# Kernel optimization log

Measured on AMD Instinct MI355X. Metric: run time of the kernel, lower is better.

Reference implementation:

```python
import jax, jax.numpy as jnp
import numpy as np

# ---- real Clebsch-Gordon tensors (Wigner 3j up to norm/sign) via equivariance null-space ----
def _su2_gens(l):
    m = np.arange(-l, l + 1)
    Lz = np.diag(m).astype(complex)
    c = np.sqrt(l * (l + 1) - m[:-1] * (m[:-1] + 1))
    Lp = np.zeros((2 * l + 1, 2 * l + 1), complex)
    Lp[np.arange(1, 2 * l + 1), np.arange(2 * l)] = c
    Lm = Lp.conj().T
    return (Lp + Lm) / 2, (Lp - Lm) / 2j, Lz

def _q_real(l):
    # complex -> real spherical-harmonic change of basis
    Q = np.zeros((2 * l + 1, 2 * l + 1), complex)
    s2 = np.sqrt(2.0)
    for m in range(-l, l + 1):
        i = m + l
        if m == 0:
            Q[i, l] = 1.0
        elif m > 0:
            Q[i, l + m] = (-1.0) ** m / s2
            Q[i, l - m] = 1.0 / s2
        else:
            Q[i, l + m] = 1j / s2
            Q[i, l - m] = -1j * (-1.0) ** m / s2
    return Q

def _real_gens(l):
    Q = _q_real(l)
    return [np.real(Q @ (1j * L) @ Q.conj().T) for L in _su2_gens(l)]

_CG = {}
def clebsch_gordon(l1, l2, l3):
    key = (l1, l2, l3)
    if key not in _CG:
        n1, n2, n3 = 2 * l1 + 1, 2 * l2 + 1, 2 * l3 + 1
        G = [_real_gens(l) for l in (l1, l2, l3)]
        rows = []
        for a in range(3):
            rows.append(np.kron(G[0][a], np.eye(n2 * n3))
                        + np.kron(np.eye(n1), np.kron(G[1][a], np.eye(n3)))
                        + np.kron(np.eye(n1 * n2), G[2][a]))
        _, s, Vh = np.linalg.svd(np.concatenate(rows, 0))
        v = Vh[-1]  # unique invariant vector (unit norm)
        if v[np.argmax(np.abs(v))] < 0:
            v = -v
        _CG[key] = v.reshape(n1, n2, n3).astype(np.float32)
    return _CG[key]

# ---- static irreps configuration (mul, degree l, parity p) ----
TP_L = [(32, 0, 1), (32, 1, -1)]
TP_R = [(32, 0, 1), (32, 1, -1)]
IRREPS_IN = [(128, 0, 1), (128, 1, -1), (128, 1, 1), (128, 2, 1)]
B = 8192
D_IN = sum(m * (2 * l + 1) for m, l, _ in IRREPS_IN)  # 1536

def _key(l, p):
    return f"{l}{'e' if p == 1 else 'o'}"

def _build_out_irreps():
    mul, order = {}, []
    for ml, ll, pl in TP_L:
        for mr, lr, pr in TP_R:
            p = pl * pr
            for l in range(abs(ll - lr), ll + lr + 1):
                k = _key(l, p)
                if k not in mul:
                    mul[k] = 0
                    order.append((l, p))
                mul[k] += ml * mr
    return [(mul[_key(l, p)], l, p) for (l, p) in order]

IRREPS_OUT = _build_out_irreps()  # [(2048,0,1),(2048,1,-1),(1024,1,1),(1024,2,1)]

def _build_schedule():
    # replicates the original's tail-consuming slice logic per (pair, output irrep)
    starts, off = [], 0
    for mul, l, p in IRREPS_OUT:
        starts.append(off)
        off += mul * (2 * l + 1)
    rem = {_key(l, p): mul for mul, l, p in IRREPS_OUT}
    sched = []
    for ml, ll, pl in TP_L:
        for mr, lr, pr in TP_R:
            mul = ml * mr
            terms = []
            for i, (mo, l, p) in enumerate(IRREPS_OUT):
                if p != pl * pr or not (abs(ll - lr) <= l <= ll + lr):
                    continue
                k = _key(l, p)
                stop = starts[i] + rem[k] * (2 * l + 1)
                start = stop - mul * (2 * l + 1)
                rem[k] -= mul
                terms.append((start, stop, l, clebsch_gordon(ll, lr, l)))
            sched.append((ml, ll, mr, lr, terms))
    assert all(v == 0 for v in rem.values())
    return sched, off

SCHEDULE, D_OUT = _build_schedule()  # D_OUT == 16384

def setup_inputs() -> dict:
    key = jax.random.key(0)
    ks = jax.random.split(key, 5)
    x = jax.random.normal(ks[0], (B, D_IN), jnp.float32)
    w_0e = jax.random.normal(ks[1], (128, 2048), jnp.float32) / np.sqrt(128.0)
    w_1o = jax.random.normal(ks[2], (128, 2048), jnp.float32) / np.sqrt(128.0)
    w_1e = jax.random.normal(ks[3], (128, 1024), jnp.float32) / np.sqrt(128.0)
    w_2e = jax.random.normal(ks[4], (128, 1024), jnp.float32) / np.sqrt(128.0)
    return {"x": x, "w_0e": w_0e, "w_1o": w_1o, "w_1e": w_1e, "w_2e": w_2e}

def _linear(x, ws):
    # e3nn-style PointwiseLinear: mix multiplicities within each irrep type
    in_off, off = {}, 0
    for m, l, p in IRREPS_IN:
        in_off[_key(l, p)] = (off, m)
        off += m * (2 * l + 1)
    outs = []
    for (mo, l, p), w in zip(IRREPS_OUT, ws):
        o, mi = in_off[_key(l, p)]
        d = 2 * l + 1
        xi = x[:, o:o + mi * d].reshape(-1, mi, d)  # [B, mul_in, 2l+1]
        yo = jnp.einsum('bui,uv->bvi', xi, w)       # [B, mul_out, 2l+1]
        outs.append(yo.reshape(xi.shape[0], mo * d))
    return jnp.concatenate(outs, axis=1)  # [B, D_OUT]

def reference(x, w_0e, w_1o, w_1e, w_2e):
    y = _linear(x, (w_0e, w_1o, w_1e, w_2e))
    blocks = []
    for ml, ll, mr, lr, terms in SCHEDULE:
        acc = None
        for start, stop, l, cg in terms:
            a = y[:, start:stop].reshape(-1, ml, mr, 2 * l + 1)  # [B,mul_l,mul_r,2l+1]
            t = jnp.einsum('bmni,lri->bmlnr', a, jnp.asarray(cg))
            acc = t if acc is None else acc + t  # [B,mul_l,2ll+1,mul_r,2lr+1]
        blocks.append(acc.reshape(acc.shape[0], -1))
    return jnp.concatenate(blocks, axis=1)  # [B, 16384]
```

## Files before the change

### kernel.cpp

```cpp
#include <hip/hip_runtime.h>


typedef __attribute__((ext_vector_type(8))) __bf16 bf16x8;
typedef __attribute__((ext_vector_type(8))) unsigned short u16x8;
typedef __attribute__((ext_vector_type(4))) float f32x4;
typedef __attribute__((ext_vector_type(2))) float f32x2;

#define A_V8_TOTAL (12 * 512 * 4 * 64)
#define B_V8_TOTAL (384 * 4 * 64)
#define P_STRIDE   (512 * 4 * 64)
#define WS_NEED_BYTES ((size_t)(A_V8_TOTAL + B_V8_TOTAL) * 16)

__device__ __forceinline__ unsigned short f2bf(float f) {
  unsigned u = __builtin_bit_cast(unsigned, f);
  u = (u + 0x7FFFu + ((u >> 16) & 1u)) >> 16;
  return (unsigned short)u;
}

__device__ __forceinline__ f32x4 mfma16(bf16x8 a, bf16x8 b, f32x4 c) {
  return __builtin_amdgcn_mfma_f32_16x16x32_bf16(a, b, c, 0, 0, 0);
}
__device__ __forceinline__ bf16x8 asbf(u16x8 v) { return __builtin_bit_cast(bf16x8, v); }
__device__ __forceinline__ void stnt(float* p, float v) { __builtin_nontemporal_store(v, p); }
__device__ __forceinline__ void stnt2(float* p, float a, float b) {
  f32x2 v; v[0] = a; v[1] = b;
  __builtin_nontemporal_store(v, (f32x2*)p);
}

__device__ __forceinline__ void gload_lds16(const void* g, void* s) {
  __builtin_amdgcn_global_load_lds((const __attribute__((address_space(1))) void*)g,
                                   (__attribute__((address_space(3))) void*)s, 16, 0, 0);
}

__global__ __launch_bounds__(256) void prep_kernel(
    const float* __restrict__ x, const float* __restrict__ w0e,
    const float* __restrict__ w1o, const float* __restrict__ w1e,
    const float* __restrict__ w2e, u16x8* __restrict__ ws) {
  int t = blockIdx.x * 256 + threadIdx.x;
  if (t < A_V8_TOTAL) {
    int l = t & 63;
    int kb = (t >> 6) & 3;
    int mt = (t >> 8) & 511;
    int p = t >> 17;
    int m = mt * 16 + (l & 15);
    int k0 = kb * 32 + (l >> 4) * 8;
    int base, d, comp;
    if (p == 0)      { base = 0;   d = 1; comp = 0;     }
    else if (p < 4)  { base = 128; d = 3; comp = p - 1; }
    else if (p < 7)  { base = 512; d = 3; comp = p - 4; }
    else             { base = 896; d = 5; comp = p - 7; }
    const float* xr = x + (size_t)m * 1536 + base + comp + k0 * d;
    u16x8 v;
#pragma unroll
    for (int e = 0; e < 8; ++e) v[e] = f2bf(xr[e * d]);
    ws[t] = v;
  } else {
    int tb = t - A_V8_TOTAL;
    if (tb >= B_V8_TOTAL) return;
    int l = tb & 63;
    int kb = (tb >> 6) & 3;
    int ci = tb >> 8;
    const float* w; int N, v0;
    if (ci < 128)      { w = w0e; N = 2048; v0 = ci * 16;         }
    else if (ci < 256) { w = w1o; N = 2048; v0 = (ci - 128) * 16; }
    else if (ci < 320) { w = w1e; N = 1024; v0 = (ci - 256) * 16; }
    else               { w = w2e; N = 1024; v0 = (ci - 320) * 16; }
    int n = v0 + (l & 15);
    int k0 = kb * 32 + (l >> 4) * 8;
    u16x8 v;
#pragma unroll
    for (int e = 0; e < 8; ++e) v[e] = f2bf(w[(size_t)(k0 + e) * N + n]);
    ws[A_V8_TOTAL + tb] = v;
  }
}

#define CLS_OF(p) ((p) == 0 ? 0 : (p) < 4 ? 1 : (p) < 7 ? 2 : 3)

__global__ __launch_bounds__(256) void tp_main(const u16x8* __restrict__ ws,
                                               float* __restrict__ out) {
  __shared__ __align__(16) u16x8 Ash[2][1536];
  const int tid = threadIdx.x;
  const int l = tid & 63;
  const int wv = tid >> 6;
  const int bid = blockIdx.x;
  const int logical = (bid & 7) * 768 + (bid >> 3);
  const int mt2 = logical / 24;
  const int sub = logical - mt2 * 24;
  const int l15 = l & 15, lhi = l >> 4;
  const u16x8* Ap = ws;
  const u16x8* Bp = ws + A_V8_TOTAL;
  const bool isL = sub < 8;
  const int nstage = isL ? 6 : 2;

  const float c3  = 0.57735026918962576f;
  const float c6  = 0.40824829046386302f;
  const float c10 = 0.31622776601683794f;
  const float c30 = 0.18257418583505537f;

  auto stageA = [&](int kb, int buf) {
    for (int i = 0; i < nstage; ++i) {
      const int e = i * 256 + tid;
      const int p = e >> 7, mfi = (e >> 6) & 1;
      const u16x8* src = Ap + (size_t)p * P_STRIDE +
                         (((((mt2 << 1) | mfi) << 2) + kb) << 6) + (e & 63);
      gload_lds16(src, &Ash[buf][i * 256 + (tid & 192)]);
    }
  };

  stageA(0, 0);

  if (isL) {
    const int vq = sub * 4 + wv;
    f32x4 acc[2][2][12];
#pragma unroll
    for (int mf = 0; mf < 2; ++mf)
#pragma unroll
      for (int vh = 0; vh < 2; ++vh)
#pragma unroll
        for (int p = 0; p < 12; ++p) acc[mf][vh][p] = (f32x4)(0.0f);

    int buf = 0;
#pragma unroll
    for (int kb = 0; kb < 4; ++kb) {
      __syncthreads();
      if (kb < 3) stageA(kb + 1, buf ^ 1);
      bf16x8 b[2][4];
#pragma unroll
      for (int vh = 0; vh < 2; ++vh) {
        const int vt = vq * 2 + vh;
        b[vh][0] = asbf(Bp[(((vt)       << 2) + kb) * 64 + l]);
        b[vh][1] = asbf(Bp[(((128 + vt) << 2) + kb) * 64 + l]);
        b[vh][2] = asbf(Bp[(((256 + vt) << 2) + kb) * 64 + l]);
        b[vh][3] = asbf(Bp[(((320 + vt) << 2) + kb) * 64 + l]);
      }
#pragma unroll
      for (int mf = 0; mf < 2; ++mf) {
        const u16x8* af = &Ash[buf][mf * 64 + l];
#pragma unroll
        for (int p = 0; p < 12; ++p) {
          const bf16x8 a = asbf(af[p * 128]);
          acc[mf][0][p] = mfma16(a, b[0][CLS_OF(p)], acc[mf][0][p]);
          acc[mf][1][p] = mfma16(a, b[1][CLS_OF(p)], acc[mf][1][p]);
        }
      }
      buf ^= 1;
    }
    const int v5 = vq;
#pragma unroll
    for (int vh = 0; vh < 2; ++vh) {
      const int v31 = (vh << 4) | l15;
#pragma unroll
      for (int mf = 0; mf < 2; ++mf) {
#pragma unroll
        for (int j = 0; j < 4; ++j) {
          const int m = mt2 * 32 + mf * 16 + lhi * 4 + j;
          float* orow = out + (size_t)m * 16384;
          float* oc = orow + 4096 + v5 * 96 + v31;
          stnt(oc + 0,  acc[mf][vh][1][j] * c3);
          stnt(oc + 32, acc[mf][vh][2][j] * c3);
          stnt(oc + 64, acc[mf][vh][3][j] * c3);
          const float s  = acc[mf][vh][0][j] * c3;
          const float e0 = acc[mf][vh][4][j], e1 = acc[mf][vh][5][j], e2 = acc[mf][vh][6][j];
          const float q0 = acc[mf][vh][7][j], q1 = acc[mf][vh][8][j];
          const float q2 = acc[mf][vh][9][j], q3 = acc[mf][vh][10][j], q4 = acc[mf][vh][11][j];
          float* od = orow + 7168 + v5 * 288 + v31 * 3;
          stnt2(od + 0,   s - q2 * c30 - q4 * c10,
                          -e2 * c6 + q1 * c10);
          stnt (od + 2,   e1 * c6 + q0 * c10);
          stnt2(od + 96,  e2 * c6 + q1 * c10,
                          s + 2.0f * q2 * c30);
          stnt (od + 98,  -e0 * c6 + q3 * c10);
          stnt2(od + 192, -e1 * c6 + q0 * c10,
                          e0 * c6 + q3 * c10);
          stnt (od + 194, s - q2 * c30 + q4 * c10);
        }
      }
    }
  } else {
    const int vtp = (sub - 8) * 4 + wv;
    f32x4 acc[2][4];
#pragma unroll
    for (int mf = 0; mf < 2; ++mf)
#pragma unroll
      for (int p = 0; p < 4; ++p) acc[mf][p] = (f32x4)(0.0f);

    const int ci0 = 64 + vtp, ci1 = 192 + vtp;
    int buf = 0;
#pragma unroll
    for (int kb = 0; kb < 4; ++kb) {
      __syncthreads();
      if (kb < 3) stageA(kb + 1, buf ^ 1);
      bf16x8 b0 = asbf(Bp[((ci0 << 2) + kb) * 64 + l]);
      bf16x8 b1 = asbf(Bp[((ci1 << 2) + kb) * 64 + l]);
#pragma unroll
      for (int mf = 0; mf < 2; ++mf) {
        const u16x8* af = &Ash[buf][mf * 64 + l];
        acc[mf][0] = mfma16(asbf(af[0 * 128]), b0, acc[mf][0]);
        acc[mf][1] = mfma16(asbf(af[1 * 128]), b1, acc[mf][1]);
        acc[mf][2] = mfma16(asbf(af[2 * 128]), b1, acc[mf][2]);
        acc[mf][3] = mfma16(asbf(af[3 * 128]), b1, acc[mf][3]);
      }
      buf ^= 1;
    }
    const int vp = vtp * 16 + l15;
#pragma unroll
    for (int mf = 0; mf < 2; ++mf) {
#pragma unroll
      for (int j = 0; j < 4; ++j) {
        const int m = mt2 * 32 + mf * 16 + lhi * 4 + j;
        float* orow = out + (size_t)m * 16384;
        stnt(orow + vp, acc[mf][0][j]);
        float* ob = orow + 1024 + vp * 3;
        stnt2(ob + 0, acc[mf][1][j] * c3, acc[mf][2][j] * c3);
        stnt (ob + 2, acc[mf][3][j] * c3);
      }
    }
  }
}

extern "C" void kernel_launch(void* const* d_in, const int* in_sizes, int n_in,
                              void* d_out, int out_size, void* d_ws, size_t ws_size,
                              hipStream_t stream) {
  if (ws_size < WS_NEED_BYTES) return;
  const float* x   = (const float*)d_in[0];
  const float* w0e = (const float*)d_in[1];
  const float* w1o = (const float*)d_in[2];
  const float* w1e = (const float*)d_in[3];
  const float* w2e = (const float*)d_in[4];
  u16x8* ws = (u16x8*)d_ws;
  float* out = (float*)d_out;

  prep_kernel<<<6528, 256, 0, stream>>>(x, w0e, w1o, w1e, w2e, ws);
  tp_main<<<6144, 256, 0, stream>>>(ws, out);
}
```

Before: 145.0 us.

## Merge light and heavy tensor-product work into each block, cut grid to 2048

Each block used to run either the heavy l=1 output path or the light path (0e/1o outputs), chosen by sub-index across 6144 blocks. Now every block runs the heavy path and then the light path for the same row tile, and the light path doubles its per-wave column width to two vh halves. The intent is to remove the load imbalance between block types and reduce launch and A-staging count. The cost is longer blocks with more sequential work, re-staging of A for the second phase, and possibly higher register pressure.

After: 150.3 us. 1.04x slower.

```diff
diff --git a/kernel.cpp b/kernel.cpp
--- a/kernel.cpp
+++ b/kernel.cpp
@@ -83,21 +83,19 @@
   const int l = tid & 63;
   const int wv = tid >> 6;
   const int bid = blockIdx.x;
-  const int logical = (bid & 7) * 768 + (bid >> 3);
-  const int mt2 = logical / 24;
-  const int sub = logical - mt2 * 24;
+  const int logical = (bid & 7) * 256 + (bid >> 3);
+  const int mt2 = logical >> 3;
+  const int vq = ((logical & 7) << 2) | wv;
   const int l15 = l & 15, lhi = l >> 4;
   const u16x8* Ap = ws;
   const u16x8* Bp = ws + A_V8_TOTAL;
-  const bool isL = sub < 8;
-  const int nstage = isL ? 6 : 2;
 
   const float c3  = 0.57735026918962576f;
   const float c6  = 0.40824829046386302f;
   const float c10 = 0.31622776601683794f;
   const float c30 = 0.18257418583505537f;
 
-  auto stageA = [&](int kb, int buf) {
+  auto stageA = [&](int kb, int buf, int nstage) {
     for (int i = 0; i < nstage; ++i) {
       const int e = i * 256 + tid;
       const int p = e >> 7, mfi = (e >> 6) & 1;
@@ -107,10 +105,8 @@
     }
   };
 
-  stageA(0, 0);
-
-  if (isL) {
-    const int vq = sub * 4 + wv;
+  {
+    stageA(0, 0, 6);
     f32x4 acc[2][2][12];
 #pragma unroll
     for (int mf = 0; mf < 2; ++mf)
@@ -123,7 +119,7 @@
 #pragma unroll
     for (int kb = 0; kb < 4; ++kb) {
       __syncthreads();
-      if (kb < 3) stageA(kb + 1, buf ^ 1);
+      if (kb < 3) stageA(kb + 1, buf ^ 1, 6);
       bf16x8 b[2][4];
 #pragma unroll
       for (int vh = 0; vh < 2; ++vh) {
@@ -176,43 +172,61 @@
         }
       }
     }
-  } else {
-    const int vtp = (sub - 8) * 4 + wv;
-    f32x4 acc[2][4];
+  }
+
+  {
+    stageA(0, 0, 2);
+    f32x4 hacc[2][2][4];
 #pragma unroll
     for (int mf = 0; mf < 2; ++mf)
 #pragma unroll
-      for (int p = 0; p < 4; ++p) acc[mf][p] = (f32x4)(0.0f);
-
-    const int ci0 = 64 + vtp, ci1 = 192 + vtp;
+      for (int vh = 0; vh < 2; ++vh)
+#pragma unroll
+        for (int p = 0; p < 4; ++p) hacc[mf][vh][p] = (f32x4)(0.0f);
+
     int buf = 0;
 #pragma unroll
     for (int kb = 0; kb < 4; ++kb) {
       __syncthreads();
-      if (kb < 3) stageA(kb + 1, buf ^ 1);
-      bf16x8 b0 = asbf(Bp[((ci0 << 2) + kb) * 64 + l]);
-      bf16x8 b1 = asbf(Bp[((ci1 << 2) + kb) * 64 + l]);
+      if (kb < 3) stageA(kb + 1, buf ^ 1, 2);
+      bf16x8 b0[2], b1[2];
+#pragma unroll
+      for (int vh = 0; vh < 2; ++vh) {
+        const int vtp = vq * 2 + vh;
+        b0[vh] = asbf(Bp[(((64 + vtp)  << 2) + kb) * 64 + l]);
+        b1[vh] = asbf(Bp[(((192 + vtp) << 2) + kb) * 64 + l]);
+      }
 #pragma unroll
       for (int mf = 0; mf < 2; ++mf) {
         const u16x8* af = &Ash[buf][mf * 64 + l];
-        acc[mf][0] = mfma16(asbf(af[0 * 128]), b0, acc[mf][0]);
-        acc[mf][1] = mfma16(asbf(af[1 * 128]), b1, acc[mf][1]);
-        acc[mf][2] = mfma16(asbf(af[2 * 128]), b1, acc[mf][2]);
-        acc[mf][3] = mfma16(asbf(af[3 * 128]), b1, acc[mf][3]);
+        const bf16x8 a0 = asbf(af[0 * 128]);
+        const bf16x8 a1 = asbf(af[1 * 128]);
+        const bf16x8 a2 = asbf(af[2 * 128]);
+        const bf16x8 a3 = asbf(af[3 * 128]);
+#pragma unroll
+        for (int vh = 0; vh < 2; ++vh) {
+          hacc[mf][vh][0] = mfma16(a0, b0[vh], hacc[mf][vh][0]);
+          hacc[mf][vh][1] = mfma16(a1, b1[vh], hacc[mf][vh][1]);
+          hacc[mf][vh][2] = mfma16(a2, b1[vh], hacc[mf][vh][2]);
+          hacc[mf][vh][3] = mfma16(a3, b1[vh], hacc[mf][vh][3]);
+        }
       }
       buf ^= 1;
     }
-    const int vp = vtp * 16 + l15;
-#pragma unroll
-    for (int mf = 0; mf < 2; ++mf) {
-#pragma unroll
-      for (int j = 0; j < 4; ++j) {
-        const int m = mt2 * 32 + mf * 16 + lhi * 4 + j;
-        float* orow = out + (size_t)m * 16384;
-        stnt(orow + vp, acc[mf][0][j]);
-        float* ob = orow + 1024 + vp * 3;
-        stnt2(ob + 0, acc[mf][1][j] * c3, acc[mf][2][j] * c3);
-        stnt (ob + 2, acc[mf][3][j] * c3);
+#pragma unroll
+    for (int vh = 0; vh < 2; ++vh) {
+      const int vp = (vq * 2 + vh) * 16 + l15;
+#pragma unroll
+      for (int mf = 0; mf < 2; ++mf) {
+#pragma unroll
+        for (int j = 0; j < 4; ++j) {
+          const int m = mt2 * 32 + mf * 16 + lhi * 4 + j;
+          float* orow = out + (size_t)m * 16384;
+          stnt(orow + vp, hacc[mf][vh][0][j]);
+          float* ob = orow + 1024 + vp * 3;
+          stnt2(ob + 0, hacc[mf][vh][1][j] * c3, hacc[mf][vh][2][j] * c3);
+          stnt (ob + 2, hacc[mf][vh][3][j] * c3);
+        }
       }
     }
   }
@@ -231,5 +245,5 @@
   float* out = (float*)d_out;
 
   prep_kernel<<<6528, 256, 0, stream>>>(x, w0e, w1o, w1e, w2e, ws);
-  tp_main<<<6144, 256, 0, stream>>>(ws, out);
-}
+  tp_main<<<2048, 256, 0, stream>>>(ws, out);
+}
```
